# Performance work log

Hardware: AMD Instinct MI355X
Metric: run time of the kernel (lower is better)

The kernel has to match this reference:

```python
import jax, jax.numpy as jnp
import numpy as np

N = 20000      # nodes
E = 640000     # edges (avg degree 32)
K = 4          # eigenvectors (sign-invariant batch axis)
HID = 64       # hidden_dim
EDIM = 32      # edge_dim == GINE out_channels
ODIM = 64      # out_dim of rho
EPS = 0.0      # GINEConv eps (default, not learned here)


def setup_inputs() -> dict:
    key = jax.random.key(0)
    ks = jax.random.split(key, 20)
    def g(i, shape):
        return jax.random.normal(ks[i], shape, dtype=jnp.float32) / np.float32(np.sqrt(shape[0]))
    inp = {}
    inp["x"] = jax.random.normal(ks[0], (K, N, 1), dtype=jnp.float32)
    inp["edge_attr"] = jax.random.normal(ks[1], (E, EDIM), dtype=jnp.float32)
    inp["edge_index"] = jax.random.randint(ks[2], (2, E), 0, N, dtype=jnp.int32)
    in_dims = [1, HID, HID]
    out_dims = [HID, HID, EDIM]
    i = 3
    for l in range(3):
        inp[f"l{l}_We"] = g(i, (EDIM, in_dims[l])); i += 1
        inp[f"l{l}_be"] = jnp.zeros((in_dims[l],), jnp.float32)
        inp[f"l{l}_W1"] = g(i, (in_dims[l], HID)); i += 1
        inp[f"l{l}_b1"] = jnp.zeros((HID,), jnp.float32)
        inp[f"l{l}_W2"] = g(i, (HID, out_dims[l])); i += 1
        inp[f"l{l}_b2"] = jnp.zeros((out_dims[l],), jnp.float32)
    inp["Wr1"] = g(i, (EDIM, HID)); i += 1
    inp["br1"] = jnp.zeros((HID,), jnp.float32)
    inp["Wr2"] = g(i, (HID, ODIM)); i += 1
    inp["br2"] = jnp.zeros((ODIM,), jnp.float32)
    return inp


def _gine_conv(h, src, dst, edge_attr, We, be, W1, b1, W2, b2):
    # h: [K, N, F_in]; edge linear maps edge features into node feature space
    e_emb = edge_attr @ We + be                      # [E, F_in]
    msg = jax.nn.relu(h[:, src, :] + e_emb)          # [K, E, F_in] gather
    agg = jax.vmap(lambda m: jax.ops.segment_sum(m, dst, num_segments=N))(msg)  # [K, N, F_in] scatter-add
    z = (1.0 + EPS) * h + agg
    return jax.nn.relu(z @ W1 + b1) @ W2 + b2        # per-layer MLP


def _phi(h, src, dst, edge_attr, layers):
    n = len(layers)
    for l, p in enumerate(layers):
        h = _gine_conv(h, src, dst, edge_attr, *p)
        if l < n - 1:
            h = jax.nn.relu(h)
    return h  # [K, N, EDIM]


def reference(x, edge_attr, edge_index,
              l0_We, l0_be, l0_W1, l0_b1, l0_W2, l0_b2,
              l1_We, l1_be, l1_W1, l1_b1, l1_W2, l1_b2,
              l2_We, l2_be, l2_W1, l2_b1, l2_W2, l2_b2,
              Wr1, br1, Wr2, br2):
    src = edge_index[0]
    dst = edge_index[1]
    layers = [
        (l0_We, l0_be, l0_W1, l0_b1, l0_W2, l0_b2),
        (l1_We, l1_be, l1_W1, l1_b1, l1_W2, l1_b2),
        (l2_We, l2_be, l2_W1, l2_b1, l2_W2, l2_b2),
    ]
    # sign invariance: phi(x) + phi(-x)
    phi_out = _phi(x, src, dst, edge_attr, layers) + _phi(-x, src, dst, edge_attr, layers)
    pooled = jnp.sum(phi_out, axis=0)                # sum over K eigenvectors -> [N, EDIM]
    return jax.nn.relu(pooled @ Wr1 + br1) @ Wr2 + br2  # rho MLP -> [N, ODIM]
```

## Files before the change

kernel.cpp:

```cpp
#include <hip/hip_runtime.h>

#define NN 20000
#define NE 640000
#define NCH 8
#define HID 64
#define EDIM 32
#define ODIM 64

typedef __attribute__((ext_vector_type(8))) short bf16x8;
typedef __attribute__((ext_vector_type(4))) float f32x4;

__device__ __forceinline__ float b2f(unsigned short u) {
    unsigned v = ((unsigned)u) << 16;
    return __builtin_bit_cast(float, v);
}
__device__ __forceinline__ unsigned short f2b(float f) {
    unsigned u = __builtin_bit_cast(unsigned, f);
    unsigned r = (u + 0x7fffu + ((u >> 16) & 1u)) >> 16;
    return (unsigned short)r;
}
__device__ __forceinline__ f32x4 mfma16(bf16x8 a, bf16x8 b, f32x4 c) {
    return __builtin_amdgcn_mfma_f32_16x16x32_bf16(a, b, c, 0, 0, 0);
}
__device__ __forceinline__ bf16x8 load_bfrag(const unsigned short* W, int ldn, int k0, int n0, int lane) {
    int g = lane >> 4, r = lane & 15;
    bf16x8 f;
#pragma unroll
    for (int j = 0; j < 8; ++j) f[j] = (short)W[(k0 + 8 * g + j) * ldn + n0 + r];
    return f;
}

__global__ __launch_bounds__(256) void k_prep(
    const float* We1, const float* We2, const float* W11, const float* W21,
    const float* W12, const float* W22, const float* W20, const float* Wr1,
    const float* Wr2, unsigned short* bw)
{
    int gid = blockIdx.x * 256 + threadIdx.x;
    const float* src; int off;
    if      (gid < 2048)  { src = We1; off = 0; }
    else if (gid < 4096)  { src = We2; off = 2048; }
    else if (gid < 8192)  { src = W11; off = 4096; }
    else if (gid < 12288) { src = W21; off = 8192; }
    else if (gid < 16384) { src = W12; off = 12288; }
    else if (gid < 18432) { src = W22; off = 16384; }
    else if (gid < 22528) { src = W20; off = 18432; }
    else if (gid < 24576) { src = Wr1; off = 22528; }
    else                  { src = Wr2; off = 24576; }
    bw[gid] = f2b(src[gid - off]);
}

__global__ __launch_bounds__(256) void k_hist(const int* __restrict__ ei, int* __restrict__ cnt)
{
    int e = blockIdx.x * 256 + threadIdx.x;
    if (e < NE) atomicAdd(&cnt[ei[NE + e]], 1);
}

__global__ __launch_bounds__(512) void k_scan(const int* __restrict__ cnt,
                                              int* __restrict__ row, int* __restrict__ cursor)
{
    __shared__ int part[512];
    int t = threadIdx.x;
    int base = t * 40;
    int s = 0;
#pragma unroll
    for (int i = 0; i < 40; ++i) { int idx = base + i; if (idx < NN) s += cnt[idx]; }
    part[t] = s;
    __syncthreads();
    int v = s;
    for (int off = 1; off < 512; off <<= 1) {
        int add = (t >= off) ? part[t - off] : 0;
        __syncthreads();
        v += add;
        part[t] = v;
        __syncthreads();
    }
    int run = v - s;
    for (int i = 0; i < 40; ++i) {
        int idx = base + i;
        if (idx < NN) { row[idx] = run; cursor[idx] = run; run += cnt[idx]; }
    }
    if (t == 511) row[NN] = NE;
}

__global__ __launch_bounds__(256) void k_scatter(const int* __restrict__ ei,
                                                 int* __restrict__ cursor, int2* __restrict__ se)
{
    int e = blockIdx.x * 256 + threadIdx.x;
    if (e < NE) {
        int d = ei[NE + e];
        int pos = atomicAdd(&cursor[d], 1);
        se[pos] = make_int2(ei[e], e);
    }
}

__global__ __launch_bounds__(256) void k_permea(
    const float* __restrict__ ea, const int2* __restrict__ se,
    const float* __restrict__ We0, const float* __restrict__ be0,
    unsigned short* __restrict__ eap, float* __restrict__ emb0)
{
    int p = blockIdx.x * 256 + threadIdx.x;
    if (p >= NE) return;
    int eid = se[p].y;
    const f32x4* s4 = (const f32x4*)(ea + (size_t)eid * 32);
    float e0 = be0[0];
#pragma unroll
    for (int h = 0; h < 4; ++h) {
        f32x4 a = s4[2 * h], b = s4[2 * h + 1];
        bf16x8 o;
#pragma unroll
        for (int j = 0; j < 4; ++j) {
            e0 = fmaf(a[j], We0[h * 8 + j], e0);
            e0 = fmaf(b[j], We0[h * 8 + 4 + j], e0);
            o[j] = (short)f2b(a[j]);
            o[4 + j] = (short)f2b(b[j]);
        }
        *(bf16x8*)(eap + (size_t)p * 32 + h * 8) = o;
    }
    emb0[p] = e0;
}

__global__ __launch_bounds__(256) void k_xt(const float* __restrict__ x, float* __restrict__ xt)
{
    int n = blockIdx.x * 256 + threadIdx.x;
    if (n < NN) {
        f32x4 v = {x[n], x[NN + n], x[2 * NN + n], x[3 * NN + n]};
        *(f32x4*)(xt + (size_t)n * 4) = v;
    }
}

__global__ __launch_bounds__(256) void k_l0_gather(
    const float* __restrict__ xt, const int2* __restrict__ se,
    const int* __restrict__ row, const float* __restrict__ emb0,
    float* __restrict__ z0)
{
    int gid = blockIdx.x * 256 + threadIdx.x;
    if (gid >= NN * NCH) return;
    int d = gid >> 3, c = gid & 7;
    int k = c & 3;
    float sgn = (c >= 4) ? -1.f : 1.f;
    float acc = 0.f;
    int p1 = row[d + 1];
    for (int p = row[d]; p < p1; ++p) {
        float xs = xt[(size_t)se[p].x * 4 + k];
        acc += fmaxf(sgn * xs + emb0[p], 0.f);
    }
    z0[gid] = sgn * xt[(size_t)d * 4 + k] + acc;
}

__global__ __launch_bounds__(256) void k_l0_mlp(
    const float* __restrict__ z0,
    const float* __restrict__ W1, const float* __restrict__ b1,
    const unsigned short* __restrict__ W2b, const float* __restrict__ b2,
    unsigned short* __restrict__ hT)
{
    constexpr int S = 72;
    __shared__ short lds[4][16 * S];
    int lane = threadIdx.x & 63, wid = threadIdx.x >> 6, g = lane >> 4, r = lane & 15;
    short* L = lds[wid];
    bf16x8 w2f[2][4];
#pragma unroll
    for (int kk = 0; kk < 2; ++kk)
#pragma unroll
        for (int t = 0; t < 4; ++t) w2f[kk][t] = load_bfrag(W2b, 64, kk * 32, t * 16, lane);
    float b2v[4];
#pragma unroll
    for (int t = 0; t < 4; ++t) b2v[t] = b2[t * 16 + r];
    float w1a[8], w1b[8], b1a[8], b1b[8];
#pragma unroll
    for (int j = 0; j < 8; ++j) {
        w1a[j] = W1[8 * g + j];      b1a[j] = b1[8 * g + j];
        w1b[j] = W1[32 + 8 * g + j]; b1b[j] = b1[32 + 8 * g + j];
    }
    int tile = blockIdx.x * 4 + wid;
    int row0 = tile * 16;
    float zv = z0[row0 + r];
    bf16x8 a0, a1;
#pragma unroll
    for (int j = 0; j < 8; ++j) {
        a0[j] = (short)f2b(fmaxf(fmaf(zv, w1a[j], b1a[j]), 0.f));
        a1[j] = (short)f2b(fmaxf(fmaf(zv, w1b[j], b1b[j]), 0.f));
    }
    f32x4 c2[4];
#pragma unroll
    for (int t = 0; t < 4; ++t) {
        f32x4 c = {0.f, 0.f, 0.f, 0.f};
        c = mfma16(a0, w2f[0][t], c);
        c = mfma16(a1, w2f[1][t], c);
        c2[t] = c;
    }
#pragma unroll
    for (int t = 0; t < 4; ++t)
#pragma unroll
        for (int i = 0; i < 4; ++i)
            L[(4 * g + i) * S + t * 16 + r] = (short)f2b(fmaxf(c2[t][i] + b2v[t], 0.f));
    asm volatile("" ::: "memory");
    int node0 = tile * 2;
#pragma unroll
    for (int half = 0; half < 2; ++half) {
        bf16x8 v;
#pragma unroll
        for (int c = 0; c < 8; ++c) v[c] = L[(half * 8 + c) * S + lane];
        *(bf16x8*)(hT + (size_t)(node0 + half) * 512 + lane * 8) = v;
    }
}

__global__ __launch_bounds__(256) void k_gather_f(
    const int2* __restrict__ se, const int* __restrict__ row,
    const unsigned short* __restrict__ eap,
    const unsigned short* __restrict__ Web, const float* __restrict__ be,
    const unsigned short* __restrict__ hT, unsigned short* __restrict__ z)
{
    constexpr int S = 72;
    __shared__ short lds[4][16 * S];
    int lane = threadIdx.x & 63, wid = threadIdx.x >> 6, g = lane >> 4, r = lane & 15;
    short* L = lds[wid];
    bf16x8 wf[4];
#pragma unroll
    for (int t = 0; t < 4; ++t) wf[t] = load_bfrag(Web, 64, 0, t * 16, lane);
    float bev[4];
#pragma unroll
    for (int t = 0; t < 4; ++t) bev[t] = be[t * 16 + r];

    int d = blockIdx.x * 4 + wid;
    int p0 = row[d], p1 = row[d + 1];
    float acc[NCH];
#pragma unroll
    for (int c = 0; c < NCH; ++c) acc[c] = 0.f;

    for (int p = p0; p < p1; p += 16) {
        int pp = p + r;
        if (pp >= p1) pp = p1 - 1;
        bf16x8 af = *(const bf16x8*)(eap + (size_t)pp * 32 + 8 * g);
        int sv = se[pp].x;
        f32x4 c[4];
#pragma unroll
        for (int t = 0; t < 4; ++t) {
            f32x4 cc = {0.f, 0.f, 0.f, 0.f};
            c[t] = mfma16(af, wf[t], cc);
        }
#pragma unroll
        for (int t = 0; t < 4; ++t)
#pragma unroll
            for (int i = 0; i < 4; ++i)
                L[(4 * g + i) * S + t * 16 + r] = (short)f2b(c[t][i] + bev[t]);
        asm volatile("" ::: "memory");
        int ne = p1 - p; if (ne > 16) ne = 16;
        for (int q = 0; q < ne; ++q) {
            int src = __shfl(sv, q, 64);
            float em = b2f((unsigned short)L[q * S + lane]);
            bf16x8 hv = *(const bf16x8*)(hT + (size_t)src * 512 + lane * 8);
#pragma unroll
            for (int c2 = 0; c2 < NCH; ++c2)
                acc[c2] += fmaxf(b2f((unsigned short)hv[c2]) + em, 0.f);
        }
        asm volatile("" ::: "memory");
    }

    bf16x8 hd = *(const bf16x8*)(hT + (size_t)d * 512 + lane * 8);
#pragma unroll
    for (int c2 = 0; c2 < NCH; ++c2)
        z[((size_t)d * 8 + c2) * 64 + lane] = f2b(b2f((unsigned short)hd[c2]) + acc[c2]);
}

template <int OUT, bool RELU2, bool TOHT>
__global__ __launch_bounds__(256) void k_mlp(
    const unsigned short* __restrict__ z,
    const unsigned short* __restrict__ W1b, const float* __restrict__ b1,
    const unsigned short* __restrict__ W2b, const float* __restrict__ b2,
    unsigned short* __restrict__ hout)
{
    constexpr int S1 = 72;
    constexpr int S2 = (OUT == 64) ? 72 : 40;
    constexpr int NT2 = OUT / 16;
    __shared__ short lds[4][16 * S1];
    int lane = threadIdx.x & 63, wid = threadIdx.x >> 6, g = lane >> 4, r = lane & 15;
    short* L = lds[wid];

    bf16x8 w1f[2][4];
#pragma unroll
    for (int kk = 0; kk < 2; ++kk)
#pragma unroll
        for (int t = 0; t < 4; ++t) w1f[kk][t] = load_bfrag(W1b, 64, kk * 32, t * 16, lane);
    bf16x8 w2f[2][NT2];
#pragma unroll
    for (int kk = 0; kk < 2; ++kk)
#pragma unroll
        for (int t = 0; t < NT2; ++t) w2f[kk][t] = load_bfrag(W2b, OUT, kk * 32, t * 16, lane);
    float b1v[4], b2v[NT2];
#pragma unroll
    for (int t = 0; t < 4; ++t) b1v[t] = b1[t * 16 + r];
#pragma unroll
    for (int t = 0; t < NT2; ++t) b2v[t] = b2[t * 16 + r];

    int tile = blockIdx.x * 4 + wid;
    int row0 = tile * 16;

    bf16x8 a0 = *(const bf16x8*)(z + (size_t)(row0 + r) * 64 + 8 * g);
    bf16x8 a1 = *(const bf16x8*)(z + (size_t)(row0 + r) * 64 + 32 + 8 * g);
    f32x4 c1[4];
#pragma unroll
    for (int t = 0; t < 4; ++t) {
        f32x4 c = {0.f, 0.f, 0.f, 0.f};
        c = mfma16(a0, w1f[0][t], c);
        c = mfma16(a1, w1f[1][t], c);
        c1[t] = c;
    }
#pragma unroll
    for (int t = 0; t < 4; ++t)
#pragma unroll
        for (int i = 0; i < 4; ++i)
            L[(4 * g + i) * S1 + t * 16 + r] = (short)f2b(fmaxf(c1[t][i] + b1v[t], 0.f));
    asm volatile("" ::: "memory");
    bf16x8 t0 = *(const bf16x8*)(L + r * S1 + 8 * g);
    bf16x8 t1 = *(const bf16x8*)(L + r * S1 + 32 + 8 * g);
    f32x4 c2[NT2];
#pragma unroll
    for (int t = 0; t < NT2; ++t) {
        f32x4 c = {0.f, 0.f, 0.f, 0.f};
        c = mfma16(t0, w2f[0][t], c);
        c = mfma16(t1, w2f[1][t], c);
        c2[t] = c;
    }
    asm volatile("" ::: "memory");
#pragma unroll
    for (int t = 0; t < NT2; ++t)
#pragma unroll
        for (int i = 0; i < 4; ++i) {
            float v = c2[t][i] + b2v[t];
            if (RELU2) v = fmaxf(v, 0.f);
            L[(4 * g + i) * S2 + t * 16 + r] = (short)f2b(v);
        }
    asm volatile("" ::: "memory");
    if (TOHT) {
        int node0 = tile * 2;
#pragma unroll
        for (int half = 0; half < 2; ++half) {
            bf16x8 v;
#pragma unroll
            for (int c = 0; c < 8; ++c) v[c] = L[(half * 8 + c) * S2 + lane];
            *(bf16x8*)(hout + (size_t)(node0 + half) * 512 + lane * 8) = v;
        }
    } else {
        bf16x8 o0 = *(const bf16x8*)(L + r * S2 + 8 * g);
        *(bf16x8*)(hout + (size_t)(row0 + r) * OUT + 8 * g) = o0;
    }
}

__global__ __launch_bounds__(256) void k_rho(
    const unsigned short* __restrict__ h2,
    const unsigned short* __restrict__ Wr1b, const float* __restrict__ br1,
    const unsigned short* __restrict__ Wr2b, const float* __restrict__ br2,
    float* __restrict__ out)
{
    constexpr int S = 72;
    __shared__ short lds[4][16 * S];
    int lane = threadIdx.x & 63, wid = threadIdx.x >> 6, g = lane >> 4, r = lane & 15;
    short* L = lds[wid];
    int tile = blockIdx.x * 4 + wid;
    if (tile * 16 >= NN) return;
    bf16x8 w1f[4], w2f[2][4];
#pragma unroll
    for (int t = 0; t < 4; ++t) w1f[t] = load_bfrag(Wr1b, 64, 0, t * 16, lane);
#pragma unroll
    for (int kk = 0; kk < 2; ++kk)
#pragma unroll
        for (int t = 0; t < 4; ++t) w2f[kk][t] = load_bfrag(Wr2b, 64, kk * 32, t * 16, lane);
    float b1v[4], b2v[4];
#pragma unroll
    for (int t = 0; t < 4; ++t) { b1v[t] = br1[t * 16 + r]; b2v[t] = br2[t * 16 + r]; }

    int n = tile * 16 + r;
    float s[8] = {0.f, 0.f, 0.f, 0.f, 0.f, 0.f, 0.f, 0.f};
#pragma unroll
    for (int c = 0; c < NCH; ++c) {
        bf16x8 hv = *(const bf16x8*)(h2 + ((size_t)n * 8 + c) * 32 + 8 * g);
#pragma unroll
        for (int j = 0; j < 8; ++j) s[j] += b2f((unsigned short)hv[j]);
    }
    bf16x8 af;
#pragma unroll
    for (int j = 0; j < 8; ++j) af[j] = (short)f2b(s[j]);
    f32x4 c1[4];
#pragma unroll
    for (int t = 0; t < 4; ++t) {
        f32x4 c = {0.f, 0.f, 0.f, 0.f};
        c1[t] = mfma16(af, w1f[t], c);
    }
#pragma unroll
    for (int t = 0; t < 4; ++t)
#pragma unroll
        for (int i = 0; i < 4; ++i)
            L[(4 * g + i) * S + t * 16 + r] = (short)f2b(fmaxf(c1[t][i] + b1v[t], 0.f));
    asm volatile("" ::: "memory");
    bf16x8 t0 = *(const bf16x8*)(L + r * S + 8 * g);
    bf16x8 t1 = *(const bf16x8*)(L + r * S + 32 + 8 * g);
    f32x4 c2[4];
#pragma unroll
    for (int t = 0; t < 4; ++t) {
        f32x4 c = {0.f, 0.f, 0.f, 0.f};
        c = mfma16(t0, w2f[0][t], c);
        c = mfma16(t1, w2f[1][t], c);
        c2[t] = c;
    }
    int nb = tile * 16;
#pragma unroll
    for (int t = 0; t < 4; ++t)
#pragma unroll
        for (int i = 0; i < 4; ++i)
            out[(size_t)(nb + 4 * g + i) * 64 + t * 16 + r] = c2[t][i] + b2v[t];
}

extern "C" void kernel_launch(void* const* d_in, const int* in_sizes, int n_in,
                              void* d_out, int out_size, void* d_ws, size_t ws_size,
                              hipStream_t stream)
{
    const float* x   = (const float*)d_in[0];
    const float* ea  = (const float*)d_in[1];
    const int*   ei  = (const int*)d_in[2];
    const float* We0 = (const float*)d_in[3];
    const float* be0 = (const float*)d_in[4];
    const float* W10 = (const float*)d_in[5];
    const float* b10 = (const float*)d_in[6];
    const float* W20 = (const float*)d_in[7];
    const float* b20 = (const float*)d_in[8];
    const float* We1 = (const float*)d_in[9];
    const float* be1 = (const float*)d_in[10];
    const float* W11 = (const float*)d_in[11];
    const float* b11 = (const float*)d_in[12];
    const float* W21 = (const float*)d_in[13];
    const float* b21 = (const float*)d_in[14];
    const float* We2 = (const float*)d_in[15];
    const float* be2 = (const float*)d_in[16];
    const float* W12 = (const float*)d_in[17];
    const float* b12 = (const float*)d_in[18];
    const float* W22 = (const float*)d_in[19];
    const float* b22 = (const float*)d_in[20];
    const float* Wr1 = (const float*)d_in[21];
    const float* br1 = (const float*)d_in[22];
    const float* Wr2 = (const float*)d_in[23];
    const float* br2 = (const float*)d_in[24];
    float* out = (float*)d_out;

    char* base = (char*)d_ws;
    unsigned short* hT   = (unsigned short*)base; base += (size_t)NN * 512 * 2;
    unsigned short* z    = (unsigned short*)base; base += (size_t)160000 * 64 * 2;
    unsigned short* h2   = (unsigned short*)base; base += (size_t)160000 * 32 * 2;
    unsigned short* eap  = (unsigned short*)base; base += (size_t)NE * 32 * 2;
    float* emb0          = (float*)base;          base += (size_t)NE * 4;
    float* z0            = (float*)base;          base += (size_t)160000 * 4;
    float* xt            = (float*)base;          base += (size_t)NN * 4 * 4;
    int2* se             = (int2*)base;           base += (size_t)NE * 8;
    int* row             = (int*)base;            base += 80128;
    int* cnt             = (int*)base;            base += 80128;
    int* cursor          = (int*)base;            base += 80128;
    unsigned short* bw   = (unsigned short*)base;

    const unsigned short* bWe1 = bw;
    const unsigned short* bWe2 = bw + 2048;
    const unsigned short* bW11 = bw + 4096;
    const unsigned short* bW21 = bw + 8192;
    const unsigned short* bW12 = bw + 12288;
    const unsigned short* bW22 = bw + 16384;
    const unsigned short* bW20 = bw + 18432;
    const unsigned short* bWr1 = bw + 22528;
    const unsigned short* bWr2 = bw + 24576;

    k_prep<<<112, 256, 0, stream>>>(We1, We2, W11, W21, W12, W22, W20, Wr1, Wr2, bw);
    hipMemsetAsync(cnt, 0, NN * sizeof(int), stream);
    k_hist<<<NE / 256, 256, 0, stream>>>(ei, cnt);
    k_scan<<<1, 512, 0, stream>>>(cnt, row, cursor);
    k_scatter<<<NE / 256, 256, 0, stream>>>(ei, cursor, se);
    k_permea<<<NE / 256, 256, 0, stream>>>(ea, se, We0, be0, eap, emb0);
    k_xt<<<(NN + 255) / 256, 256, 0, stream>>>(x, xt);

    k_l0_gather<<<(NN * NCH) / 256, 256, 0, stream>>>(xt, se, row, emb0, z0);
    k_l0_mlp<<<2500, 256, 0, stream>>>(z0, W10, b10, bW20, b20, hT);

    k_gather_f<<<NN / 4, 256, 0, stream>>>(se, row, eap, bWe1, be1, hT, z);
    k_mlp<64, true, true><<<2500, 256, 0, stream>>>(z, bW11, b11, bW21, b21, hT);

    k_gather_f<<<NN / 4, 256, 0, stream>>>(se, row, eap, bWe2, be2, hT, z);
    k_mlp<32, false, false><<<2500, 256, 0, stream>>>(z, bW12, b12, bW22, b22, h2);

    k_rho<<<313, 256, 0, stream>>>(h2, bWr1, br1, bWr2, br2, out);
}
```

Baseline: 420.2 us.

## Split edge arrays, prefetch next edge chunk, unroll gather with fp32 LDS embeddings

The interleaved (src, eid) edge array becomes two separate int arrays, so gather kernels read only the source indices. The layer-0 gather computes the +x and -x sign branches in one thread, sharing loads across them. k_gather_f now prefetches the next 16-edge chunk's features and source indices while the current chunk's MFMA runs. The bias is folded into the MFMA accumulator, edge embeddings are kept in fp32 in LDS, and the inner edge loop is fully unrolled to 16 with -inf padding so masked edges add nothing. This removes load latency and loop overhead, at the cost of redundant hT loads on partial chunks and more LDS.

```diff
diff --git a/kernel.cpp b/kernel.cpp
--- a/kernel.cpp
+++ b/kernel.cpp
@@ -83,24 +83,26 @@
 }
 
 __global__ __launch_bounds__(256) void k_scatter(const int* __restrict__ ei,
-                                                 int* __restrict__ cursor, int2* __restrict__ se)
+                                                 int* __restrict__ cursor,
+                                                 int* __restrict__ srcp, int* __restrict__ eidp)
 {
     int e = blockIdx.x * 256 + threadIdx.x;
     if (e < NE) {
         int d = ei[NE + e];
         int pos = atomicAdd(&cursor[d], 1);
-        se[pos] = make_int2(ei[e], e);
+        srcp[pos] = ei[e];
+        eidp[pos] = e;
     }
 }
 
 __global__ __launch_bounds__(256) void k_permea(
-    const float* __restrict__ ea, const int2* __restrict__ se,
+    const float* __restrict__ ea, const int* __restrict__ eidp,
     const float* __restrict__ We0, const float* __restrict__ be0,
     unsigned short* __restrict__ eap, float* __restrict__ emb0)
 {
     int p = blockIdx.x * 256 + threadIdx.x;
     if (p >= NE) return;
-    int eid = se[p].y;
+    int eid = eidp[p];
     const f32x4* s4 = (const f32x4*)(ea + (size_t)eid * 32);
     float e0 = be0[0];
 #pragma unroll
@@ -129,22 +131,24 @@
 }
 
 __global__ __launch_bounds__(256) void k_l0_gather(
-    const float* __restrict__ xt, const int2* __restrict__ se,
+    const float* __restrict__ xt, const int* __restrict__ srcp,
     const int* __restrict__ row, const float* __restrict__ emb0,
     float* __restrict__ z0)
 {
     int gid = blockIdx.x * 256 + threadIdx.x;
-    if (gid >= NN * NCH) return;
-    int d = gid >> 3, c = gid & 7;
-    int k = c & 3;
-    float sgn = (c >= 4) ? -1.f : 1.f;
-    float acc = 0.f;
+    if (gid >= NN * 4) return;
+    int d = gid >> 2, k = gid & 3;
+    float accp = 0.f, accm = 0.f;
     int p1 = row[d + 1];
     for (int p = row[d]; p < p1; ++p) {
-        float xs = xt[(size_t)se[p].x * 4 + k];
-        acc += fmaxf(sgn * xs + emb0[p], 0.f);
-    }
-    z0[gid] = sgn * xt[(size_t)d * 4 + k] + acc;
+        float xs = xt[(size_t)srcp[p] * 4 + k];
+        float e0 = emb0[p];
+        accp += fmaxf(xs + e0, 0.f);
+        accm += fmaxf(e0 - xs, 0.f);
+    }
+    float xd = xt[(size_t)d * 4 + k];
+    z0[d * 8 + k] = xd + accp;
+    z0[d * 8 + k + 4] = accm - xd;
 }
 
 __global__ __launch_bounds__(256) void k_l0_mlp(
@@ -205,15 +209,15 @@
 }
 
 __global__ __launch_bounds__(256) void k_gather_f(
-    const int2* __restrict__ se, const int* __restrict__ row,
+    const int* __restrict__ srcp, const int* __restrict__ row,
     const unsigned short* __restrict__ eap,
     const unsigned short* __restrict__ Web, const float* __restrict__ be,
     const unsigned short* __restrict__ hT, unsigned short* __restrict__ z)
 {
-    constexpr int S = 72;
-    __shared__ short lds[4][16 * S];
+    constexpr int S4 = 66;
+    __shared__ float lds[4][16 * S4];
     int lane = threadIdx.x & 63, wid = threadIdx.x >> 6, g = lane >> 4, r = lane & 15;
-    short* L = lds[wid];
+    float* L = lds[wid];
     bf16x8 wf[4];
 #pragma unroll
     for (int t = 0; t < 4; ++t) wf[t] = load_bfrag(Web, 64, 0, t * 16, lane);
@@ -227,39 +231,66 @@
 #pragma unroll
     for (int c = 0; c < NCH; ++c) acc[c] = 0.f;
 
+    bf16x8 afc = {0,0,0,0,0,0,0,0};
+    int svc = 0;
+    if (p0 < p1) {
+        int pp = p0 + r; if (pp > p1 - 1) pp = p1 - 1;
+        afc = *(const bf16x8*)(eap + (size_t)pp * 32 + 8 * g);
+        svc = srcp[pp];
+    }
+
     for (int p = p0; p < p1; p += 16) {
-        int pp = p + r;
-        if (pp >= p1) pp = p1 - 1;
-        bf16x8 af = *(const bf16x8*)(eap + (size_t)pp * 32 + 8 * g);
-        int sv = se[pp].x;
+        int ne = p1 - p; if (ne > 16) ne = 16;
         f32x4 c[4];
 #pragma unroll
         for (int t = 0; t < 4; ++t) {
-            f32x4 cc = {0.f, 0.f, 0.f, 0.f};
-            c[t] = mfma16(af, wf[t], cc);
+            f32x4 cc = {bev[t], bev[t], bev[t], bev[t]};
+            c[t] = mfma16(afc, wf[t], cc);
         }
+        bf16x8 afn = afc; int svn = svc;
+        int pn = p + 16;
+        if (pn < p1) {
+            int ppn = pn + r; if (ppn > p1 - 1) ppn = p1 - 1;
+            afn = *(const bf16x8*)(eap + (size_t)ppn * 32 + 8 * g);
+            svn = srcp[ppn];
+        }
 #pragma unroll
         for (int t = 0; t < 4; ++t)
 #pragma unroll
-            for (int i = 0; i < 4; ++i)
-                L[(4 * g + i) * S + t * 16 + r] = (short)f2b(c[t][i] + bev[t]);
+            for (int i = 0; i < 4; ++i) {
+                float v = (4 * g + i < ne) ? c[t][i] : -__builtin_inff();
+                L[(4 * g + i) * S4 + t * 16 + r] = v;
+            }
         asm volatile("" ::: "memory");
-        int ne = p1 - p; if (ne > 16) ne = 16;
-        for (int q = 0; q < ne; ++q) {
-            int src = __shfl(sv, q, 64);
-            float em = b2f((unsigned short)L[q * S + lane]);
-            bf16x8 hv = *(const bf16x8*)(hT + (size_t)src * 512 + lane * 8);
-#pragma unroll
-            for (int c2 = 0; c2 < NCH; ++c2)
-                acc[c2] += fmaxf(b2f((unsigned short)hv[c2]) + em, 0.f);
+#pragma unroll
+        for (int q = 0; q < 16; ++q) {
+            int src = __builtin_amdgcn_readlane(svc, q);
+            float em = L[q * S4 + lane];
+            uint4 hv = *(const uint4*)(hT + (size_t)src * 512 + (lane << 3));
+            unsigned dw0 = hv.x, dw1 = hv.y, dw2 = hv.z, dw3 = hv.w;
+            acc[0] += fmaxf(__builtin_bit_cast(float, dw0 << 16) + em, 0.f);
+            acc[1] += fmaxf(__builtin_bit_cast(float, dw0 & 0xffff0000u) + em, 0.f);
+            acc[2] += fmaxf(__builtin_bit_cast(float, dw1 << 16) + em, 0.f);
+            acc[3] += fmaxf(__builtin_bit_cast(float, dw1 & 0xffff0000u) + em, 0.f);
+            acc[4] += fmaxf(__builtin_bit_cast(float, dw2 << 16) + em, 0.f);
+            acc[5] += fmaxf(__builtin_bit_cast(float, dw2 & 0xffff0000u) + em, 0.f);
+            acc[6] += fmaxf(__builtin_bit_cast(float, dw3 << 16) + em, 0.f);
+            acc[7] += fmaxf(__builtin_bit_cast(float, dw3 & 0xffff0000u) + em, 0.f);
         }
         asm volatile("" ::: "memory");
-    }
-
-    bf16x8 hd = *(const bf16x8*)(hT + (size_t)d * 512 + lane * 8);
-#pragma unroll
-    for (int c2 = 0; c2 < NCH; ++c2)
-        z[((size_t)d * 8 + c2) * 64 + lane] = f2b(b2f((unsigned short)hd[c2]) + acc[c2]);
+        afc = afn; svc = svn;
+    }
+
+    uint4 hd = *(const uint4*)(hT + (size_t)d * 512 + (lane << 3));
+    unsigned hw[4] = {hd.x, hd.y, hd.z, hd.w};
+    unsigned short* zd = z + (size_t)d * 8 * 64 + lane;
+#pragma unroll
+    for (int j = 0; j < 4; ++j) {
+        float lo = __builtin_bit_cast(float, hw[j] << 16);
+        float hi = __builtin_bit_cast(float, hw[j] & 0xffff0000u);
+        zd[(2 * j) * 64] = f2b(lo + acc[2 * j]);
+        zd[(2 * j + 1) * 64] = f2b(hi + acc[2 * j + 1]);
+    }
 }
 
 template <int OUT, bool RELU2, bool TOHT>
@@ -449,7 +480,8 @@
     float* emb0          = (float*)base;          base += (size_t)NE * 4;
     float* z0            = (float*)base;          base += (size_t)160000 * 4;
     float* xt            = (float*)base;          base += (size_t)NN * 4 * 4;
-    int2* se             = (int2*)base;           base += (size_t)NE * 8;
+    int* srcp            = (int*)base;            base += (size_t)NE * 4;
+    int* eidp            = (int*)base;            base += (size_t)NE * 4;
     int* row             = (int*)base;            base += 80128;
     int* cnt             = (int*)base;            base += 80128;
     int* cursor          = (int*)base;            base += 80128;
@@ -469,17 +501,17 @@
     hipMemsetAsync(cnt, 0, NN * sizeof(int), stream);
     k_hist<<<NE / 256, 256, 0, stream>>>(ei, cnt);
     k_scan<<<1, 512, 0, stream>>>(cnt, row, cursor);
-    k_scatter<<<NE / 256, 256, 0, stream>>>(ei, cursor, se);
-    k_permea<<<NE / 256, 256, 0, stream>>>(ea, se, We0, be0, eap, emb0);
+    k_scatter<<<NE / 256, 256, 0, stream>>>(ei, cursor, srcp, eidp);
+    k_permea<<<NE / 256, 256, 0, stream>>>(ea, eidp, We0, be0, eap, emb0);
     k_xt<<<(NN + 255) / 256, 256, 0, stream>>>(x, xt);
 
-    k_l0_gather<<<(NN * NCH) / 256, 256, 0, stream>>>(xt, se, row, emb0, z0);
+    k_l0_gather<<<(NN * 4 + 255) / 256, 256, 0, stream>>>(xt, srcp, row, emb0, z0);
     k_l0_mlp<<<2500, 256, 0, stream>>>(z0, W10, b10, bW20, b20, hT);
 
-    k_gather_f<<<NN / 4, 256, 0, stream>>>(se, row, eap, bWe1, be1, hT, z);
+    k_gather_f<<<NN / 4, 256, 0, stream>>>(srcp, row, eap, bWe1, be1, hT, z);
     k_mlp<64, true, true><<<2500, 256, 0, stream>>>(z, bW11, b11, bW21, b21, hT);
 
-    k_gather_f<<<NN / 4, 256, 0, stream>>>(se, row, eap, bWe2, be2, hT, z);
+    k_gather_f<<<NN / 4, 256, 0, stream>>>(srcp, row, eap, bWe2, be2, hT, z);
     k_mlp<32, false, false><<<2500, 256, 0, stream>>>(z, bW12, b12, bW22, b22, h2);
 
     k_rho<<<313, 256, 0, stream>>>(h2, bWr1, br1, bWr2, br2, out);
```

Result: faster. 404.9 us (-3.7%).
